# Optimization experiments

Hardware: AMD Instinct MI355X
Metric: run time of the kernel (lower is better)

## Reference

```python
import jax, jax.numpy as jnp
import numpy as np

WD = 11
HF = WD // 2  # 5

def _offsets():
    # Reproduce the torch module's expanding-ring offset ordering exactly.
    offs = []
    for i in range(1, HF + 1):
        for v in range(HF - i, HF + i + 1):
            for u in range(HF - i, HF + i + 1):
                if not (u == HF and v == HF) and (u, v) not in offs:
                    offs.append((u, v))
    return offs  # length WD*WD-1 = 120

_OFFS = _offsets()


def setup_inputs() -> dict:
    key = jax.random.key(0)
    x = jax.random.normal(key, (2, 3, 384, 1280), dtype=jnp.float32)
    return {"x": x, "attack": 1}


def reference(x, attack):
    n, c, h, w = x.shape
    xm = jnp.mean(x, axis=1)  # [n,h,w] grayscale
    xp = jnp.pad(xm, ((0, 0), (HF, HF), (HF, HF)), mode="reflect")  # [n,h+2*HF,w+2*HF]
    # All 120 shifted views in ring order; static slices, stacked on channel dim.
    shifted = jnp.stack([xp[:, v:v + h, u:u + w] for (u, v) in _OFFS], axis=1)  # [n,120,h,w]
    center = xm[:, None, :, :]
    if attack:
        return jax.nn.sigmoid((shifted - center) * 100000.0)
    return shifted >= center
```

## Files before the change

kernel.cpp:

```cpp
#include <hip/hip_runtime.h>
#include <cstddef>
#include <cstdint>

constexpr int N_  = 2;
constexpr int C_  = 3;
constexpr int H_  = 384;
constexpr int W_  = 1280;
constexpr int HWp = H_ * W_;
constexpr int NOFF = 120;
constexpr int HF_  = 5;

__host__ __device__ constexpr int k_of(int u, int v) {
    int du = u - HF_, dv = v - HF_;
    int au = du < 0 ? -du : du;
    int av = dv < 0 ? -dv : dv;
    int r = au > av ? au : av;
    if (r == 0) return -1;
    int base = (2 * r - 1) * (2 * r - 1) - 1;
    int dv2 = v - (HF_ - r);
    int du2 = u - (HF_ - r);
    int idx = 0;
    if (dv2 == 0)            idx = du2;
    else if (dv2 == 2 * r)   idx = (2 * r + 1) + 2 * (2 * r - 1) + du2;
    else                     idx = (2 * r + 1) + 2 * (dv2 - 1) + (du2 == 0 ? 0 : 1);
    return base + idx;
}

__global__ __launch_bounds__(256) void mean_kernel(const float* __restrict__ x,
                                                   float* __restrict__ xm) {
    int i = blockIdx.x * 256 + threadIdx.x;
    constexpr int TOT4 = N_ * HWp / 4;
    if (i >= TOT4) return;
    int n = i / (HWp / 4);
    int j = i - n * (HWp / 4);
    const float4* x0 = (const float4*)(x + (size_t)n * C_ * HWp);
    const float4* x1 = (const float4*)(x + (size_t)n * C_ * HWp + HWp);
    const float4* x2 = (const float4*)(x + (size_t)n * C_ * HWp + 2 * HWp);
    float4 a = x0[j], b = x1[j], c = x2[j];
    float4 m;
    m.x = (a.x + b.x + c.x) / 3.0f;
    m.y = (a.y + b.y + c.y) / 3.0f;
    m.z = (a.z + b.z + c.z) / 3.0f;
    m.w = (a.w + b.w + c.w) / 3.0f;
    ((float4*)xm)[i] = m;
}

__device__ __forceinline__ float census_val(float s, float center) {
    float d = s - center;
    float r;
    if (__builtin_expect(fabsf(d) >= 1.6e-4f, 1)) {
        r = d > 0.0f ? 1.0f : 0.0f;
    } else {
        float e = __expf(d * -100000.0f);
        r = __builtin_amdgcn_rcpf(1.0f + e);
    }
    return r;
}

__global__ __launch_bounds__(256) void census_kernel(const float* __restrict__ xm,
                                                     float* __restrict__ out) {
    int bx = blockIdx.x % 5;
    int t  = blockIdx.x / 5;
    int y  = t % H_;
    int n  = t / H_;
    int x  = bx * 256 + threadIdx.x;

    const float* xmn = xm + (size_t)n * HWp;
    float center = xmn[y * W_ + x];

    int xr[11];
#pragma unroll
    for (int u = 0; u < 11; ++u) {
        int xx = x + u - HF_;
        xx = xx < 0 ? -xx : xx;
        xx = xx >= W_ ? 2 * (W_ - 1) - xx : xx;
        xr[u] = xx;
    }

    float* outp = out + (size_t)n * NOFF * HWp + (size_t)y * W_ + x;

#pragma unroll
    for (int v = 0; v < 11; ++v) {
        int yy = y + v - HF_;
        yy = yy < 0 ? -yy : yy;
        yy = yy >= H_ ? 2 * (H_ - 1) - yy : yy;
        const float* row = xmn + (size_t)yy * W_;
#pragma unroll
        for (int u = 0; u < 11; ++u) {
            if (u == HF_ && v == HF_) continue;
            const int k = k_of(u, v);
            float s = row[xr[u]];
            outp[(size_t)k * HWp] = census_val(s, center);
        }
    }
}

__device__ __forceinline__ float mean3(const float* __restrict__ xn, int off) {
    return (xn[off] + xn[off + HWp] + xn[off + 2 * HWp]) / 3.0f;
}

__global__ __launch_bounds__(256) void census_fused_kernel(const float* __restrict__ x,
                                                           float* __restrict__ out) {
    int bx = blockIdx.x % 5;
    int t  = blockIdx.x / 5;
    int y  = t % H_;
    int n  = t / H_;
    int xp = bx * 256 + threadIdx.x;

    const float* xn = x + (size_t)n * C_ * HWp;
    float center = mean3(xn, y * W_ + xp);

    int xr[11];
#pragma unroll
    for (int u = 0; u < 11; ++u) {
        int xx = xp + u - HF_;
        xx = xx < 0 ? -xx : xx;
        xx = xx >= W_ ? 2 * (W_ - 1) - xx : xx;
        xr[u] = xx;
    }

    float* outp = out + (size_t)n * NOFF * HWp + (size_t)y * W_ + xp;

#pragma unroll
    for (int v = 0; v < 11; ++v) {
        int yy = y + v - HF_;
        yy = yy < 0 ? -yy : yy;
        yy = yy >= H_ ? 2 * (H_ - 1) - yy : yy;
#pragma unroll
        for (int u = 0; u < 11; ++u) {
            if (u == HF_ && v == HF_) continue;
            const int k = k_of(u, v);
            float s = mean3(xn, yy * W_ + xr[u]);
            outp[(size_t)k * HWp] = census_val(s, center);
        }
    }
}

extern "C" void kernel_launch(void* const* d_in, const int* in_sizes, int n_in,
                              void* d_out, int out_size, void* d_ws, size_t ws_size,
                              hipStream_t stream) {
    const float* x = (const float*)d_in[0];
    float* out = (float*)d_out;

    const size_t xm_bytes = (size_t)N_ * HWp * sizeof(float);
    const int census_blocks = N_ * H_ * (W_ / 256);

    if (ws_size >= xm_bytes) {
        float* xm = (float*)d_ws;
        const int mean_blocks = (N_ * HWp / 4 + 255) / 256;
        mean_kernel<<<mean_blocks, 256, 0, stream>>>(x, xm);
        census_kernel<<<census_blocks, 256, 0, stream>>>(xm, out);
    } else {
        census_fused_kernel<<<census_blocks, 256, 0, stream>>>(x, out);
    }
}
```

Measured before the change: 468.5 us.

## Restructure census to one block per offset-row with float4 stores

Replaces the per-pixel kernel, which looped over all 120 offsets, with a grid of one block per (batch, offset, row). Each of 320 threads handles 4 contiguous pixels and writes a single float4. The offsets come from a constant-memory table, and the sigmoid slow path is taken once per 4-pixel group. The goal is fully coalesced, vectorised stores for the 470 MB output, at the cost of more blocks and the center row being reloaded once per offset.

```diff
diff --git a/kernel.cpp b/kernel.cpp
--- a/kernel.cpp
+++ b/kernel.cpp
@@ -10,21 +10,25 @@
 constexpr int NOFF = 120;
 constexpr int HF_  = 5;
 
-__host__ __device__ constexpr int k_of(int u, int v) {
-    int du = u - HF_, dv = v - HF_;
-    int au = du < 0 ? -du : du;
-    int av = dv < 0 ? -dv : dv;
-    int r = au > av ? au : av;
-    if (r == 0) return -1;
-    int base = (2 * r - 1) * (2 * r - 1) - 1;
-    int dv2 = v - (HF_ - r);
-    int du2 = u - (HF_ - r);
+struct OffTab { int du[NOFF]; int dv[NOFF]; };
+constexpr OffTab make_offs() {
+    OffTab t{};
     int idx = 0;
-    if (dv2 == 0)            idx = du2;
-    else if (dv2 == 2 * r)   idx = (2 * r + 1) + 2 * (2 * r - 1) + du2;
-    else                     idx = (2 * r + 1) + 2 * (dv2 - 1) + (du2 == 0 ? 0 : 1);
-    return base + idx;
+    for (int i = 1; i <= HF_; ++i)
+        for (int v = HF_ - i; v <= HF_ + i; ++v)
+            for (int u = HF_ - i; u <= HF_ + i; ++u) {
+                if (u == HF_ && v == HF_) continue;
+                int au = u < HF_ ? HF_ - u : u - HF_;
+                int av = v < HF_ ? HF_ - v : v - HF_;
+                int r = au > av ? au : av;
+                if (r != i) continue;
+                t.du[idx] = u - HF_;
+                t.dv[idx] = v - HF_;
+                ++idx;
+            }
+    return t;
 }
+__constant__ OffTab OFFS = make_offs();
 
 __global__ __launch_bounds__(256) void mean_kernel(const float* __restrict__ x,
                                                    float* __restrict__ xm) {
@@ -45,95 +49,107 @@
     ((float4*)xm)[i] = m;
 }
 
-__device__ __forceinline__ float census_val(float s, float center) {
-    float d = s - center;
-    float r;
-    if (__builtin_expect(fabsf(d) >= 1.6e-4f, 1)) {
-        r = d > 0.0f ? 1.0f : 0.0f;
-    } else {
-        float e = __expf(d * -100000.0f);
-        r = __builtin_amdgcn_rcpf(1.0f + e);
-    }
-    return r;
+__device__ __forceinline__ float sig1e5(float d) {
+    float e = __expf(d * -100000.0f);
+    return __builtin_amdgcn_rcpf(1.0f + e);
 }
 
-__global__ __launch_bounds__(256) void census_kernel(const float* __restrict__ xm,
-                                                     float* __restrict__ out) {
-    int bx = blockIdx.x % 5;
-    int t  = blockIdx.x / 5;
-    int y  = t % H_;
-    int n  = t / H_;
-    int x  = bx * 256 + threadIdx.x;
+__global__ __launch_bounds__(320) void census_rows(const float* __restrict__ xm,
+                                                   float* __restrict__ out) {
+    int b  = blockIdx.x;
+    int y  = b % H_;
+    int t2 = b / H_;
+    int k  = t2 % NOFF;
+    int n  = t2 / NOFF;
 
-    const float* xmn = xm + (size_t)n * HWp;
-    float center = xmn[y * W_ + x];
+    int du = OFFS.du[k];
+    int dv = OFFS.dv[k];
+    int yy = y + dv;
+    yy = yy < 0 ? -yy : yy;
+    yy = yy >= H_ ? 2 * (H_ - 1) - yy : yy;
 
-    int xr[11];
+    const float* cr = xm + (size_t)n * HWp + (size_t)y  * W_;
+    const float* sr = xm + (size_t)n * HWp + (size_t)yy * W_;
+
+    int x4 = (int)threadIdx.x * 4;
+    float4 c = *(const float4*)(cr + x4);
+    float cc[4] = {c.x, c.y, c.z, c.w};
+
+    float s[4];
 #pragma unroll
-    for (int u = 0; u < 11; ++u) {
-        int xx = x + u - HF_;
+    for (int j = 0; j < 4; ++j) {
+        int xx = x4 + j + du;
         xx = xx < 0 ? -xx : xx;
         xx = xx >= W_ ? 2 * (W_ - 1) - xx : xx;
-        xr[u] = xx;
+        s[j] = sr[xx];
     }
 
-    float* outp = out + (size_t)n * NOFF * HWp + (size_t)y * W_ + x;
+    float d[4], r[4];
+    bool slow = false;
+#pragma unroll
+    for (int j = 0; j < 4; ++j) {
+        d[j] = s[j] - cc[j];
+        r[j] = d[j] > 0.0f ? 1.0f : 0.0f;
+        slow |= (fabsf(d[j]) < 1.6e-4f);
+    }
+    if (__builtin_expect(slow, 0)) {
+#pragma unroll
+        for (int j = 0; j < 4; ++j) r[j] = sig1e5(d[j]);
+    }
 
-#pragma unroll
-    for (int v = 0; v < 11; ++v) {
-        int yy = y + v - HF_;
-        yy = yy < 0 ? -yy : yy;
-        yy = yy >= H_ ? 2 * (H_ - 1) - yy : yy;
-        const float* row = xmn + (size_t)yy * W_;
-#pragma unroll
-        for (int u = 0; u < 11; ++u) {
-            if (u == HF_ && v == HF_) continue;
-            const int k = k_of(u, v);
-            float s = row[xr[u]];
-            outp[(size_t)k * HWp] = census_val(s, center);
-        }
-    }
+    float4 o; o.x = r[0]; o.y = r[1]; o.z = r[2]; o.w = r[3];
+    *(float4*)(out + (size_t)n * NOFF * HWp + (size_t)k * HWp
+               + (size_t)y * W_ + x4) = o;
 }
 
 __device__ __forceinline__ float mean3(const float* __restrict__ xn, int off) {
     return (xn[off] + xn[off + HWp] + xn[off + 2 * HWp]) / 3.0f;
 }
 
-__global__ __launch_bounds__(256) void census_fused_kernel(const float* __restrict__ x,
-                                                           float* __restrict__ out) {
-    int bx = blockIdx.x % 5;
-    int t  = blockIdx.x / 5;
-    int y  = t % H_;
-    int n  = t / H_;
-    int xp = bx * 256 + threadIdx.x;
+__global__ __launch_bounds__(320) void census_rows_fused(const float* __restrict__ x,
+                                                         float* __restrict__ out) {
+    int b  = blockIdx.x;
+    int y  = b % H_;
+    int t2 = b / H_;
+    int k  = t2 % NOFF;
+    int n  = t2 / NOFF;
+
+    int du = OFFS.du[k];
+    int dv = OFFS.dv[k];
+    int yy = y + dv;
+    yy = yy < 0 ? -yy : yy;
+    yy = yy >= H_ ? 2 * (H_ - 1) - yy : yy;
 
     const float* xn = x + (size_t)n * C_ * HWp;
-    float center = mean3(xn, y * W_ + xp);
+    int x4 = (int)threadIdx.x * 4;
 
-    int xr[11];
+    float cc[4], s[4];
 #pragma unroll
-    for (int u = 0; u < 11; ++u) {
-        int xx = xp + u - HF_;
+    for (int j = 0; j < 4; ++j) cc[j] = mean3(xn, y * W_ + x4 + j);
+#pragma unroll
+    for (int j = 0; j < 4; ++j) {
+        int xx = x4 + j + du;
         xx = xx < 0 ? -xx : xx;
         xx = xx >= W_ ? 2 * (W_ - 1) - xx : xx;
-        xr[u] = xx;
+        s[j] = mean3(xn, yy * W_ + xx);
     }
 
-    float* outp = out + (size_t)n * NOFF * HWp + (size_t)y * W_ + xp;
+    float d[4], r[4];
+    bool slow = false;
+#pragma unroll
+    for (int j = 0; j < 4; ++j) {
+        d[j] = s[j] - cc[j];
+        r[j] = d[j] > 0.0f ? 1.0f : 0.0f;
+        slow |= (fabsf(d[j]) < 1.6e-4f);
+    }
+    if (__builtin_expect(slow, 0)) {
+#pragma unroll
+        for (int j = 0; j < 4; ++j) r[j] = sig1e5(d[j]);
+    }
 
-#pragma unroll
-    for (int v = 0; v < 11; ++v) {
-        int yy = y + v - HF_;
-        yy = yy < 0 ? -yy : yy;
-        yy = yy >= H_ ? 2 * (H_ - 1) - yy : yy;
-#pragma unroll
-        for (int u = 0; u < 11; ++u) {
-            if (u == HF_ && v == HF_) continue;
-            const int k = k_of(u, v);
-            float s = mean3(xn, yy * W_ + xr[u]);
-            outp[(size_t)k * HWp] = census_val(s, center);
-        }
-    }
+    float4 o; o.x = r[0]; o.y = r[1]; o.z = r[2]; o.w = r[3];
+    *(float4*)(out + (size_t)n * NOFF * HWp + (size_t)k * HWp
+               + (size_t)y * W_ + x4) = o;
 }
 
 extern "C" void kernel_launch(void* const* d_in, const int* in_sizes, int n_in,
@@ -143,14 +159,14 @@
     float* out = (float*)d_out;
 
     const size_t xm_bytes = (size_t)N_ * HWp * sizeof(float);
-    const int census_blocks = N_ * H_ * (W_ / 256);
+    const int census_blocks = N_ * NOFF * H_;
 
     if (ws_size >= xm_bytes) {
         float* xm = (float*)d_ws;
         const int mean_blocks = (N_ * HWp / 4 + 255) / 256;
         mean_kernel<<<mean_blocks, 256, 0, stream>>>(x, xm);
-        census_kernel<<<census_blocks, 256, 0, stream>>>(xm, out);
+        census_rows<<<census_blocks, 320, 0, stream>>>(xm, out);
     } else {
-        census_fused_kernel<<<census_blocks, 256, 0, stream>>>(x, out);
+        census_rows_fused<<<census_blocks, 320, 0, stream>>>(x, out);
     }
 }
```

Result: slower. 513.9 us (+9.7%).

## Process four pixels per thread with float4 nontemporal stores and register row reuse

Applied to the files above, without the earlier changes.

Each thread now handles four adjacent pixels of a row. It loads 14 neighbours per stencil row into registers and reuses them across the 11 horizontal offsets. Results go out as 16-byte nontemporal vector stores, and the sigmoid fallback is checked once per group of four. The aim is to cut store instruction count and cache pollution on the large output write. The cost is fewer blocks, one per image row, and more registers per thread.

```diff
diff --git a/kernel.cpp b/kernel.cpp
--- a/kernel.cpp
+++ b/kernel.cpp
@@ -9,6 +9,8 @@
 constexpr int HWp = H_ * W_;
 constexpr int NOFF = 120;
 constexpr int HF_  = 5;
+
+typedef float vfloat4 __attribute__((ext_vector_type(4)));
 
 __host__ __device__ constexpr int k_of(int u, int v) {
     int du = u - HF_, dv = v - HF_;
@@ -45,52 +47,57 @@
     ((float4*)xm)[i] = m;
 }
 
-__device__ __forceinline__ float census_val(float s, float center) {
-    float d = s - center;
-    float r;
-    if (__builtin_expect(fabsf(d) >= 1.6e-4f, 1)) {
-        r = d > 0.0f ? 1.0f : 0.0f;
-    } else {
-        float e = __expf(d * -100000.0f);
-        r = __builtin_amdgcn_rcpf(1.0f + e);
-    }
-    return r;
+__device__ __forceinline__ float sig1e5(float d) {
+    float e = __expf(d * -100000.0f);
+    return __builtin_amdgcn_rcpf(1.0f + e);
 }
 
-__global__ __launch_bounds__(256) void census_kernel(const float* __restrict__ xm,
-                                                     float* __restrict__ out) {
-    int bx = blockIdx.x % 5;
-    int t  = blockIdx.x / 5;
-    int y  = t % H_;
-    int n  = t / H_;
-    int x  = bx * 256 + threadIdx.x;
+__device__ __forceinline__ int reflect(int i, int n) {
+    i = i < 0 ? -i : i;
+    i = i >= n ? 2 * (n - 1) - i : i;
+    return i;
+}
+
+__global__ __launch_bounds__(320) void census_rows(const float* __restrict__ xm,
+                                                   float* __restrict__ out) {
+    int y = blockIdx.x % H_;
+    int n = blockIdx.x / H_;
+    int x4 = (int)threadIdx.x * 4;
 
     const float* xmn = xm + (size_t)n * HWp;
-    float center = xmn[y * W_ + x];
+    float4 c = *(const float4*)(xmn + (size_t)y * W_ + x4);
+    float cc[4] = {c.x, c.y, c.z, c.w};
 
-    int xr[11];
-#pragma unroll
-    for (int u = 0; u < 11; ++u) {
-        int xx = x + u - HF_;
-        xx = xx < 0 ? -xx : xx;
-        xx = xx >= W_ ? 2 * (W_ - 1) - xx : xx;
-        xr[u] = xx;
-    }
-
-    float* outp = out + (size_t)n * NOFF * HWp + (size_t)y * W_ + x;
+    float* outp = out + (size_t)n * NOFF * HWp + (size_t)y * W_ + x4;
 
 #pragma unroll
     for (int v = 0; v < 11; ++v) {
-        int yy = y + v - HF_;
-        yy = yy < 0 ? -yy : yy;
-        yy = yy >= H_ ? 2 * (H_ - 1) - yy : yy;
+        int yy = reflect(y + v - HF_, H_);
         const float* row = xmn + (size_t)yy * W_;
+
+        float sp[14];
+#pragma unroll
+        for (int m = 0; m < 14; ++m)
+            sp[m] = row[reflect(x4 - HF_ + m, W_)];
+
 #pragma unroll
         for (int u = 0; u < 11; ++u) {
             if (u == HF_ && v == HF_) continue;
             const int k = k_of(u, v);
-            float s = row[xr[u]];
-            outp[(size_t)k * HWp] = census_val(s, center);
+            float r[4];
+            bool slow = false;
+#pragma unroll
+            for (int j = 0; j < 4; ++j) {
+                float d = sp[u + j] - cc[j];
+                r[j] = d > 0.0f ? 1.0f : 0.0f;
+                slow |= (fabsf(d) < 1.6e-4f);
+            }
+            if (__builtin_expect(slow, 0)) {
+#pragma unroll
+                for (int j = 0; j < 4; ++j) r[j] = sig1e5(sp[u + j] - cc[j]);
+            }
+            vfloat4 o = {r[0], r[1], r[2], r[3]};
+            __builtin_nontemporal_store(o, (vfloat4*)(outp + (size_t)k * HWp));
         }
     }
 }
@@ -99,39 +106,45 @@
     return (xn[off] + xn[off + HWp] + xn[off + 2 * HWp]) / 3.0f;
 }
 
-__global__ __launch_bounds__(256) void census_fused_kernel(const float* __restrict__ x,
-                                                           float* __restrict__ out) {
-    int bx = blockIdx.x % 5;
-    int t  = blockIdx.x / 5;
-    int y  = t % H_;
-    int n  = t / H_;
-    int xp = bx * 256 + threadIdx.x;
+__global__ __launch_bounds__(320) void census_rows_fused(const float* __restrict__ x,
+                                                         float* __restrict__ out) {
+    int y = blockIdx.x % H_;
+    int n = blockIdx.x / H_;
+    int x4 = (int)threadIdx.x * 4;
 
     const float* xn = x + (size_t)n * C_ * HWp;
-    float center = mean3(xn, y * W_ + xp);
+    float cc[4];
+#pragma unroll
+    for (int j = 0; j < 4; ++j) cc[j] = mean3(xn, y * W_ + x4 + j);
 
-    int xr[11];
-#pragma unroll
-    for (int u = 0; u < 11; ++u) {
-        int xx = xp + u - HF_;
-        xx = xx < 0 ? -xx : xx;
-        xx = xx >= W_ ? 2 * (W_ - 1) - xx : xx;
-        xr[u] = xx;
-    }
-
-    float* outp = out + (size_t)n * NOFF * HWp + (size_t)y * W_ + xp;
+    float* outp = out + (size_t)n * NOFF * HWp + (size_t)y * W_ + x4;
 
 #pragma unroll
     for (int v = 0; v < 11; ++v) {
-        int yy = y + v - HF_;
-        yy = yy < 0 ? -yy : yy;
-        yy = yy >= H_ ? 2 * (H_ - 1) - yy : yy;
+        int yy = reflect(y + v - HF_, H_);
+        float sp[14];
+#pragma unroll
+        for (int m = 0; m < 14; ++m)
+            sp[m] = mean3(xn, yy * W_ + reflect(x4 - HF_ + m, W_));
+
 #pragma unroll
         for (int u = 0; u < 11; ++u) {
             if (u == HF_ && v == HF_) continue;
             const int k = k_of(u, v);
-            float s = mean3(xn, yy * W_ + xr[u]);
-            outp[(size_t)k * HWp] = census_val(s, center);
+            float r[4];
+            bool slow = false;
+#pragma unroll
+            for (int j = 0; j < 4; ++j) {
+                float d = sp[u + j] - cc[j];
+                r[j] = d > 0.0f ? 1.0f : 0.0f;
+                slow |= (fabsf(d) < 1.6e-4f);
+            }
+            if (__builtin_expect(slow, 0)) {
+#pragma unroll
+                for (int j = 0; j < 4; ++j) r[j] = sig1e5(sp[u + j] - cc[j]);
+            }
+            vfloat4 o = {r[0], r[1], r[2], r[3]};
+            __builtin_nontemporal_store(o, (vfloat4*)(outp + (size_t)k * HWp));
         }
     }
 }
@@ -143,14 +156,14 @@
     float* out = (float*)d_out;
 
     const size_t xm_bytes = (size_t)N_ * HWp * sizeof(float);
-    const int census_blocks = N_ * H_ * (W_ / 256);
+    const int census_blocks = N_ * H_;
 
     if (ws_size >= xm_bytes) {
         float* xm = (float*)d_ws;
         const int mean_blocks = (N_ * HWp / 4 + 255) / 256;
         mean_kernel<<<mean_blocks, 256, 0, stream>>>(x, xm);
-        census_kernel<<<census_blocks, 256, 0, stream>>>(xm, out);
+        census_rows<<<census_blocks, 320, 0, stream>>>(xm, out);
     } else {
-        census_fused_kernel<<<census_blocks, 256, 0, stream>>>(x, out);
+        census_rows_fused<<<census_blocks, 320, 0, stream>>>(x, out);
     }
 }
```

Result: no change. 470.2 us (median of 2 runs) (+0.4%).
